# Performance work log

Measured on AMD Instinct MI355X. Metric: run time of the kernel, lower is better.

Reference implementation:

```python
import jax, jax.numpy as jnp
import numpy as np

EPS = 1e-8


def setup_inputs() -> dict:
    key = jax.random.key(0)
    k_q, k_m = jax.random.split(key)
    NB = NS = 256
    B = 4096
    # regular 2D grid over [0,1]^2
    gx = jnp.linspace(0.0, 1.0, NB, dtype=jnp.float32)
    gy = jnp.linspace(0.0, 1.0, NS, dtype=jnp.float32)
    indices_2d = jnp.stack(jnp.meshgrid(gx, gy, indexing="ij"), axis=-1)  # [NB,NS,2]
    indices_db = indices_2d.reshape(-1, 2)  # [NB*NS, 2]
    grid_spacing = jnp.array([gx[1] - gx[0], gy[1] - gy[0]], dtype=jnp.float32)
    # metrics already min-max normalized to [0,1] (as _extract_relevant does)
    relevant_metrics_2d = jax.random.uniform(k_m, (NB, NS), dtype=jnp.float32)
    relevant_metrics = relevant_metrics_2d.reshape(-1)
    # queries inside the grid interior
    query_vectors = 0.05 + 0.9 * jax.random.uniform(k_q, (B, 2), dtype=jnp.float32)
    temperature = 0.1 * jnp.ones((1,), dtype=jnp.float32)
    return {
        "query_vectors": query_vectors,
        "temperature": temperature,
        "indices_db": indices_db,
        "relevant_metrics": relevant_metrics,
        "indices_2d": indices_2d,
        "relevant_metrics_2d": relevant_metrics_2d,
        "grid_spacing": grid_spacing,
        "kernel_size": 15,
    }


def round_ste(x):
    return x + jax.lax.stop_gradient(jnp.round(x) - x)


def reference(query_vectors, temperature, indices_db, relevant_metrics,
              indices_2d, relevant_metrics_2d, grid_spacing, kernel_size):
    # ---- hard_get: flat k-NN via sq-dist matmul + argmin (non-differentiable) ----
    q = jax.lax.stop_gradient(query_vectors)               # [B,2]
    q_norm = jnp.sum(q * q, axis=-1, keepdims=True)        # [B,1]
    i_norm = jnp.sum(indices_db * indices_db, axis=-1)     # [D]
    dot = q @ indices_db.T                                  # [B,D] (1 GB intermediate)
    sq_dist = q_norm + i_norm[None, :] - 2.0 * dot
    min_idx = jnp.argmin(sq_dist, axis=-1)                 # [B]
    hard = relevant_metrics[min_idx]                       # [B]

    # ---- soft_get_local: windowed softmax gather (differentiable) ----
    grid_origin = indices_2d[0, 0]                         # [2]
    qf = query_vectors
    rel_pos = (qf - grid_origin) / grid_spacing            # [B,2]
    voxel = round_ste(rel_pos).astype(jnp.int32)           # [B,2]
    radius = kernel_size // 2
    offs = jnp.arange(-radius, radius + 1, dtype=jnp.int32)
    neighbor_offsets = jnp.stack(jnp.meshgrid(offs, offs, indexing="ij"), axis=-1).reshape(-1, 2)  # [K2,2]
    coords = voxel[:, None, :] + neighbor_offsets[None, :, :]   # [B,K2,2]
    x, y = coords[..., 0], coords[..., 1]
    neighbor_xy = indices_2d[x, y]                         # [B,K2,2] (jnp clamps OOB like original)
    neighbor_metrics = relevant_metrics_2d[x, y]           # [B,K2]
    dists = jnp.sum((qf[:, None, :] - neighbor_xy) ** 2, axis=-1)  # [B,K2]
    weights = jax.nn.softmax(-dists / (temperature + EPS), axis=-1)
    soft = jnp.sum(weights * neighbor_metrics, axis=-1)    # [B]

    return jnp.stack([hard, soft])                         # [2,B]
```

## Files before the change

### kernel.cpp

```cpp
#include <hip/hip_runtime.h>


#define NG 256

__global__ void stage_axes(const float* __restrict__ idb,
                           float* __restrict__ wsx,
                           float* __restrict__ wsy) {
    int t = threadIdx.x;
    if (t < NG) {
        wsx[t] = idb[(size_t)2 * NG * t];
        wsy[t] = idb[2 * t + 1];
    }
}

__device__ __forceinline__ int clampi(int v, int lo, int hi) {
    return v < lo ? lo : (v > hi ? hi : v);
}

__global__ __launch_bounds__(256) void latent_lookup(
    const float* __restrict__ q,
    const float* __restrict__ temp,
    const float* __restrict__ metrics,
    const float* __restrict__ m2d,
    const float* __restrict__ i2d,
    const float* __restrict__ gs,
    const int*   __restrict__ ksz,
    const float* __restrict__ wsx,
    const float* __restrict__ wsy,
    float* __restrict__ out,
    int B) {
#pragma clang fp contract(off)
    int wave = (int)((blockIdx.x * blockDim.x + threadIdx.x) >> 6);
    int lane = threadIdx.x & 63;
    if (wave >= B) return;

    float qx = q[2 * wave + 0];
    float qy = q[2 * wave + 1];
    float ox = i2d[0], oy = i2d[1];
    float sx = gs[0],  sy = gs[1];

    int vx = (int)rintf((qx - ox) / sx);
    int vy = (int)rintf((qy - oy) / sy);

    int i0 = 0;
    {
        double best = 1e300;
        for (int d = -2; d <= 2; ++d) {
            int i = clampi(vx + d, 0, NG - 1);
            double dd = (double)qx - (double)wsx[i];
            dd *= dd;
            if (dd < best) { best = dd; i0 = i; }
        }
    }
    int j0 = 0;
    {
        double best = 1e300;
        for (int d = -2; d <= 2; ++d) {
            int j = clampi(vy + d, 0, NG - 1);
            double dd = (double)qy - (double)wsy[j];
            dd *= dd;
            if (dd < best) { best = dd; j0 = j; }
        }
    }

    float qxx = qx * qx;
    float qyy = qy * qy;
    float qn  = qxx + qyy;
    float bestv = 3.0e38f;
    int   besti = NG * NG;
    for (int di = -1; di <= 1; ++di) {
        int i = clampi(i0 + di, 0, NG - 1);
        float gxi = wsx[i];
        float px  = qx * gxi;
        float gxx = gxi * gxi;
        for (int dj = -1; dj <= 1; ++dj) {
            int j = clampi(j0 + dj, 0, NG - 1);
            float gyj = wsy[j];
            float dot = __builtin_fmaf(qy, gyj, px);
            float gyy = gyj * gyj;
            float inr = gxx + gyy;
            float A   = qn + inr;
            float c   = A - 2.0f * dot;
            int fd = i * NG + j;
            if (c < bestv || (c == bestv && fd < besti)) { bestv = c; besti = fd; }
        }
    }
    float hard = metrics[besti];

    int ks = ksz[0];
    int radius = ks >> 1;
    int K2 = ks * ks;
    float denom = temp[0] + 1e-8f;

    float smax = -3.0e38f;
    for (int k = lane; k < K2; k += 64) {
        int xo = k / ks - radius, yo = k % ks - radius;
        int x = clampi(vx + xo, 0, NG - 1);
        int y = clampi(vy + yo, 0, NG - 1);
        float dx = qx - wsx[x], dy = qy - wsy[y];
        float dist = dx * dx + dy * dy;
        smax = fmaxf(smax, -dist / denom);
    }
    for (int off = 32; off; off >>= 1)
        smax = fmaxf(smax, __shfl_xor(smax, off, 64));

    float se = 0.0f, sem = 0.0f;
    for (int k = lane; k < K2; k += 64) {
        int xo = k / ks - radius, yo = k % ks - radius;
        int x = clampi(vx + xo, 0, NG - 1);
        int y = clampi(vy + yo, 0, NG - 1);
        float dx = qx - wsx[x], dy = qy - wsy[y];
        float dist = dx * dx + dy * dy;
        float e = expf(-dist / denom - smax);
        se  += e;
        sem += e * m2d[x * NG + y];
    }
    for (int off = 32; off; off >>= 1) {
        se  += __shfl_xor(se,  off, 64);
        sem += __shfl_xor(sem, off, 64);
    }

    if (lane == 0) {
        out[wave]     = hard;
        out[B + wave] = sem / se;
    }
}

extern "C" void kernel_launch(void* const* d_in, const int* in_sizes, int n_in,
                              void* d_out, int out_size, void* d_ws, size_t ws_size,
                              hipStream_t stream) {
    const float* q       = (const float*)d_in[0];
    const float* T       = (const float*)d_in[1];
    const float* idb     = (const float*)d_in[2];
    const float* metrics = (const float*)d_in[3];
    const float* i2d     = (const float*)d_in[4];
    const float* m2d     = (const float*)d_in[5];
    const float* gs      = (const float*)d_in[6];
    const int*   ks      = (const int*)d_in[7];
    float* out = (float*)d_out;
    int B = in_sizes[0] / 2;

    float* wsx = (float*)d_ws;
    float* wsy = wsx + NG;

    stage_axes<<<1, NG, 0, stream>>>(idb, wsx, wsy);

    int blocks = (B + 3) / 4;
    latent_lookup<<<blocks, 256, 0, stream>>>(q, T, metrics, m2d, i2d, gs, ks,
                                              wsx, wsy, out, B);
}
```

Baseline: 75.91 us.

## Fuse axis staging into main kernel via shared memory and drop per-element div/mod

Removes the separate staging kernel launch; each block now loads the 256 x and y grid axes from the flattened index database into shared memory and synchronizes before computing. The softmax window loops replace the per-iteration integer divide and modulo with incremental row/column counters, and the kernel-size and temperature loads are hoisted earlier. This cuts one launch and its dependency plus integer division cost, at the price of every block performing a strided 256-element global gather (the x-axis reads are 2 KB apart) and a barrier.

```diff
diff --git a/kernel.cpp b/kernel.cpp
--- a/kernel.cpp
+++ b/kernel.cpp
@@ -2,16 +2,6 @@
 
 
 #define NG 256
-
-__global__ void stage_axes(const float* __restrict__ idb,
-                           float* __restrict__ wsx,
-                           float* __restrict__ wsy) {
-    int t = threadIdx.x;
-    if (t < NG) {
-        wsx[t] = idb[(size_t)2 * NG * t];
-        wsy[t] = idb[2 * t + 1];
-    }
-}
 
 __device__ __forceinline__ int clampi(int v, int lo, int hi) {
     return v < lo ? lo : (v > hi ? hi : v);
@@ -20,16 +10,25 @@
 __global__ __launch_bounds__(256) void latent_lookup(
     const float* __restrict__ q,
     const float* __restrict__ temp,
+    const float* __restrict__ idb,
     const float* __restrict__ metrics,
     const float* __restrict__ m2d,
     const float* __restrict__ i2d,
     const float* __restrict__ gs,
     const int*   __restrict__ ksz,
-    const float* __restrict__ wsx,
-    const float* __restrict__ wsy,
     float* __restrict__ out,
     int B) {
 #pragma clang fp contract(off)
+    __shared__ float wsx[NG];
+    __shared__ float wsy[NG];
+
+    {
+        int t = threadIdx.x;
+        wsx[t] = idb[(size_t)2 * NG * t];
+        wsy[t] = idb[2 * t + 1];
+    }
+    __syncthreads();
+
     int wave = (int)((blockIdx.x * blockDim.x + threadIdx.x) >> 6);
     int lane = threadIdx.x & 63;
     if (wave >= B) return;
@@ -38,6 +37,8 @@
     float qy = q[2 * wave + 1];
     float ox = i2d[0], oy = i2d[1];
     float sx = gs[0],  sy = gs[1];
+    int   ks = ksz[0];
+    float denom = temp[0] + 1e-8f;
 
     int vx = (int)rintf((qx - ox) / sx);
     int vy = (int)rintf((qy - oy) / sy);
@@ -87,33 +88,37 @@
     }
     float hard = metrics[besti];
 
-    int ks = ksz[0];
     int radius = ks >> 1;
     int K2 = ks * ks;
-    float denom = temp[0] + 1e-8f;
 
     float smax = -3.0e38f;
-    for (int k = lane; k < K2; k += 64) {
-        int xo = k / ks - radius, yo = k % ks - radius;
-        int x = clampi(vx + xo, 0, NG - 1);
-        int y = clampi(vy + yo, 0, NG - 1);
-        float dx = qx - wsx[x], dy = qy - wsy[y];
-        float dist = dx * dx + dy * dy;
-        smax = fmaxf(smax, -dist / denom);
+    {
+        int xo = lane / ks, yo = lane - xo * ks;
+        for (int k = lane; k < K2; k += 64) {
+            int x = clampi(vx + xo - radius, 0, NG - 1);
+            int y = clampi(vy + yo - radius, 0, NG - 1);
+            float dx = qx - wsx[x], dy = qy - wsy[y];
+            float dist = dx * dx + dy * dy;
+            smax = fmaxf(smax, -dist / denom);
+            yo += 64; while (yo >= ks) { yo -= ks; xo += 1; }
+        }
     }
     for (int off = 32; off; off >>= 1)
         smax = fmaxf(smax, __shfl_xor(smax, off, 64));
 
     float se = 0.0f, sem = 0.0f;
-    for (int k = lane; k < K2; k += 64) {
-        int xo = k / ks - radius, yo = k % ks - radius;
-        int x = clampi(vx + xo, 0, NG - 1);
-        int y = clampi(vy + yo, 0, NG - 1);
-        float dx = qx - wsx[x], dy = qy - wsy[y];
-        float dist = dx * dx + dy * dy;
-        float e = expf(-dist / denom - smax);
-        se  += e;
-        sem += e * m2d[x * NG + y];
+    {
+        int xo = lane / ks, yo = lane - xo * ks;
+        for (int k = lane; k < K2; k += 64) {
+            int x = clampi(vx + xo - radius, 0, NG - 1);
+            int y = clampi(vy + yo - radius, 0, NG - 1);
+            float dx = qx - wsx[x], dy = qy - wsy[y];
+            float dist = dx * dx + dy * dy;
+            float e = expf(-dist / denom - smax);
+            se  += e;
+            sem += e * m2d[x * NG + y];
+            yo += 64; while (yo >= ks) { yo -= ks; xo += 1; }
+        }
     }
     for (int off = 32; off; off >>= 1) {
         se  += __shfl_xor(se,  off, 64);
@@ -140,12 +145,7 @@
     float* out = (float*)d_out;
     int B = in_sizes[0] / 2;
 
-    float* wsx = (float*)d_ws;
-    float* wsy = wsx + NG;
-
-    stage_axes<<<1, NG, 0, stream>>>(idb, wsx, wsy);
-
     int blocks = (B + 3) / 4;
-    latent_lookup<<<blocks, 256, 0, stream>>>(q, T, metrics, m2d, i2d, gs, ks,
-                                              wsx, wsy, out, B);
+    latent_lookup<<<blocks, 256, 0, stream>>>(q, T, idb, metrics, m2d, i2d, gs, ks,
+                                              out, B);
 }
```

Result: faster. 74.03 us (-2.5%).
